# Kernel tuning notes

Measured on AMD Instinct MI355X. Metric: run time of the kernel, lower is better.

The kernel has to match this reference:

```python
import jax, jax.numpy as jnp
import numpy as np

DIM = 1024
NUM_HEADS = 16
HEAD_DIM = DIM // NUM_HEADS
SCALE = HEAD_DIM ** -0.5


def setup_inputs() -> dict:
    key = jax.random.key(0)
    k1, k2, k3 = jax.random.split(key, 3)
    B, S = 2, 2048
    x = jax.random.normal(k1, (B, S, DIM), dtype=jnp.float32)
    # nn.Linear(dim, 3*dim, bias=False): store as [in, out] for x @ W
    w_qkv = jax.random.normal(k2, (DIM, 3 * DIM), dtype=jnp.float32) * (DIM ** -0.5)
    w_out = jax.random.normal(k3, (DIM, DIM), dtype=jnp.float32) * (DIM ** -0.5)
    return {"x": x, "w_qkv": w_qkv, "w_out": w_out}


def reference(x, w_qkv, w_out):
    B, S, _ = x.shape
    qkv = x @ w_qkv                               # [B,S,3*D]
    q, k, v = jnp.split(qkv, 3, axis=-1)          # each [B,S,D]
    def heads(t):
        return t.reshape(B, S, NUM_HEADS, HEAD_DIM).transpose(0, 2, 1, 3)  # [B,H,S,d]
    q, k, v = heads(q), heads(k), heads(v)
    scores = jnp.einsum('bhqd,bhkd->bhqk', q, k) * SCALE   # [B,H,S,S]
    probs = jax.nn.softmax(scores, axis=-1)
    out = jnp.einsum('bhqk,bhkd->bhqd', probs, v)          # [B,H,S,d]
    out = out.transpose(0, 2, 1, 3).reshape(B, S, DIM)
    return out @ w_out
```

## Files before the change

### kernel.cpp

```cpp
#include <hip/hip_runtime.h>


typedef __bf16 bf16x8 __attribute__((ext_vector_type(8)));
typedef __bf16 bf16x4 __attribute__((ext_vector_type(4)));
typedef float floatx4 __attribute__((ext_vector_type(4)));
typedef _Float16 f16x4 __attribute__((ext_vector_type(4)));
typedef _Float16 f16x8 __attribute__((ext_vector_type(8)));

#define MFMA16(a, b, c) __builtin_amdgcn_mfma_f32_16x16x32_bf16((a), (b), (c), 0, 0, 0)

__device__ __forceinline__ void gl_lds16(const void* g, void* l) {
  __builtin_amdgcn_global_load_lds((__attribute__((address_space(1))) void*)(g),
                                   (__attribute__((address_space(3))) void*)(l),
                                   16, 0, 0);
}

__global__ __launch_bounds__(256) void prep(const float* __restrict__ x,
                                            const float* __restrict__ w_qkv,
                                            const float* __restrict__ w_out,
                                            __bf16* __restrict__ xb,
                                            __bf16* __restrict__ wqkvt,
                                            __bf16* __restrict__ woutt) {
  __shared__ float tile[64][65];
  const int bid = blockIdx.x, t = threadIdx.x;
  if (bid < 4096) {
    int i = (bid * 256 + t) * 4;
    float4 v = *(const float4*)(x + i);
    bf16x4 o = { (__bf16)v.x, (__bf16)v.y, (__bf16)v.z, (__bf16)v.w };
    *(bf16x4*)(xb + i) = o;
    return;
  }
  const float* w;
  __bf16* wt;
  int K = 1024, N, k0, n0;
  if (bid < 4864) {
    int i = bid - 4096;
    w = w_qkv; wt = wqkvt; N = 3072; k0 = (i & 15) * 64; n0 = (i >> 4) * 64;
  } else {
    int i = bid - 4864;
    w = w_out; wt = woutt; N = 1024; k0 = (i & 15) * 64; n0 = (i >> 4) * 64;
  }
  for (int j = 0; j < 16; ++j) {
    int e = j * 256 + t, r = e >> 6, c = e & 63;
    tile[r][c] = w[(size_t)(k0 + r) * N + n0 + c];
  }
  __syncthreads();
  for (int j = 0; j < 16; ++j) {
    int e = j * 256 + t, r = e >> 6, c = e & 63;
    wt[(size_t)(n0 + r) * K + k0 + c] = (__bf16)tile[c][r];
  }
}

__global__ __launch_bounds__(256) void gemm_qkv(const __bf16* __restrict__ A,
                                                const __bf16* __restrict__ Bt,
                                                __bf16* __restrict__ qkb,
                                                __bf16* __restrict__ vt) {
  constexpr int K = 1024;
  __shared__ __align__(16) __bf16 aS[128 * 32];
  __shared__ __align__(16) __bf16 bS[128 * 32];
  const int t = threadIdx.x;
  const int lane = t & 63, wave = t >> 6;
  const int l15 = lane & 15, quad = lane >> 4;
  const int wm = wave >> 1, wn = wave & 1;
  const int m0 = blockIdx.y * 128, n0 = blockIdx.x * 128;

  const floatx4 fzero = {0.f, 0.f, 0.f, 0.f};
  floatx4 acc[4][4];
  for (int mt = 0; mt < 4; ++mt)
    for (int nt = 0; nt < 4; ++nt) acc[mt][nt] = fzero;

  const int arow = t >> 2;
  const int ach = ((t & 3) ^ (arow & 3)) * 8;
  const __bf16* gA0 = A + (size_t)(m0 + arow) * K + ach;
  const __bf16* gA1 = gA0 + (size_t)64 * K;
  const __bf16* gB0 = Bt + (size_t)(n0 + arow) * K + ach;
  const __bf16* gB1 = gB0 + (size_t)64 * K;
  const int swz = (quad ^ (l15 & 3)) * 8;

  for (int k0 = 0; k0 < K; k0 += 32) {
    __syncthreads();
    gl_lds16(gA0 + k0, (char*)aS + t * 16);
    gl_lds16(gA1 + k0, (char*)aS + 4096 + t * 16);
    gl_lds16(gB0 + k0, (char*)bS + t * 16);
    gl_lds16(gB1 + k0, (char*)bS + 4096 + t * 16);
    __syncthreads();

    bf16x8 af[4], bfr[4];
    for (int mt = 0; mt < 4; ++mt)
      af[mt] = *(const bf16x8*)(aS + (wm * 64 + mt * 16 + l15) * 32 + swz);
    for (int nt = 0; nt < 4; ++nt)
      bfr[nt] = *(const bf16x8*)(bS + (wn * 64 + nt * 16 + l15) * 32 + swz);
    for (int mt = 0; mt < 4; ++mt)
      for (int nt = 0; nt < 4; ++nt)
        acc[mt][nt] = MFMA16(af[mt], bfr[nt], acc[mt][nt]);
  }

  for (int mt = 0; mt < 4; ++mt) {
    int row = m0 + wm * 64 + mt * 16 + quad * 4;
    for (int nt = 0; nt < 4; ++nt) {
      int col0 = n0 + wn * 64 + nt * 16;
      if (col0 >= 2048) {
        int dfull = col0 + l15 - 2048;
        int bh = ((row >> 11) << 4) + (dfull >> 6);
        int d = dfull & 63, s0 = row & 2047;
        bf16x4 pk = { (__bf16)acc[mt][nt][0], (__bf16)acc[mt][nt][1],
                      (__bf16)acc[mt][nt][2], (__bf16)acc[mt][nt][3] };
        *(bf16x4*)(vt + ((size_t)bh * 64 + d) * 2048 + s0) = pk;
      } else {
        int col = col0 + l15;
        __bf16* cp = qkb + (size_t)row * 2048 + col;
        for (int r = 0; r < 4; ++r) cp[(size_t)r * 2048] = (__bf16)acc[mt][nt][r];
      }
    }
  }
}

__global__ __launch_bounds__(256) void gemm_n64(const __bf16* __restrict__ A,
                                                const __bf16* __restrict__ Bt,
                                                float* __restrict__ C) {
  constexpr int K = 1024, N = 1024;
  __shared__ __align__(16) __bf16 aS[128 * 32];
  __shared__ __align__(16) __bf16 bS[64 * 32];
  const int t = threadIdx.x;
  const int lane = t & 63, wave = t >> 6;
  const int l15 = lane & 15, quad = lane >> 4;
  const int m0 = blockIdx.y * 128, n0 = blockIdx.x * 64;

  const floatx4 fzero = {0.f, 0.f, 0.f, 0.f};
  floatx4 acc[2][4];
  for (int mt = 0; mt < 2; ++mt)
    for (int nt = 0; nt < 4; ++nt) acc[mt][nt] = fzero;

  const int arow = t >> 2;
  const int ach = ((t & 3) ^ (arow & 3)) * 8;
  const __bf16* gA0 = A + (size_t)(m0 + arow) * K + ach;
  const __bf16* gA1 = gA0 + (size_t)64 * K;
  const __bf16* gB0 = Bt + (size_t)(n0 + arow) * K + ach;
  const int swz = (quad ^ (l15 & 3)) * 8;

  for (int k0 = 0; k0 < K; k0 += 32) {
    __syncthreads();
    gl_lds16(gA0 + k0, (char*)aS + t * 16);
    gl_lds16(gA1 + k0, (char*)aS + 4096 + t * 16);
    gl_lds16(gB0 + k0, (char*)bS + t * 16);
    __syncthreads();

    bf16x8 af[2], bfr[4];
    for (int mt = 0; mt < 2; ++mt)
      af[mt] = *(const bf16x8*)(aS + (wave * 32 + mt * 16 + l15) * 32 + swz);
    for (int nt = 0; nt < 4; ++nt)
      bfr[nt] = *(const bf16x8*)(bS + (nt * 16 + l15) * 32 + swz);
    for (int mt = 0; mt < 2; ++mt)
      for (int nt = 0; nt < 4; ++nt)
        acc[mt][nt] = MFMA16(af[mt], bfr[nt], acc[mt][nt]);
  }

  for (int mt = 0; mt < 2; ++mt) {
    int row = m0 + wave * 32 + mt * 16 + quad * 4;
    for (int nt = 0; nt < 4; ++nt) {
      int col = n0 + nt * 16 + l15;
      float* cp = C + (size_t)row * N + col;
      for (int r = 0; r < 4; ++r) cp[(size_t)r * N] = acc[mt][nt][r];
    }
  }
}

__global__ __launch_bounds__(256) void flash_attn(const __bf16* __restrict__ qkb,
                                                  const __bf16* __restrict__ vt,
                                                  _Float16* __restrict__ oPart,
                                                  float* __restrict__ lPart) {
  constexpr float SCALE = 0.125f;
  __shared__ __align__(16) __bf16 kS[2 * 64 * 64];
  __shared__ __align__(16) __bf16 vS[2 * 64 * 64];
  __shared__ __align__(16) __bf16 pT[4 * 16 * 64];

  const int t = threadIdx.x;
  const int lane = t & 63, wave = t >> 6;
  const int l15 = lane & 15, quad = lane >> 4;
  const int qb = blockIdx.x, bh = blockIdx.y, grp = blockIdx.z;
  const int b = bh >> 4, h = bh & 15;

  bf16x8 qf[2][2];
  for (int qt = 0; qt < 2; ++qt) {
    const __bf16* qp = qkb +
        (size_t)(b * 2048 + qb * 128 + wave * 32 + qt * 16 + l15) * 2048 + h * 64 + quad * 8;
    qf[qt][0] = *(const bf16x8*)qp;
    qf[qt][1] = *(const bf16x8*)(qp + 32);
  }

  const floatx4 fzero = {0.f, 0.f, 0.f, 0.f};
  floatx4 oacc[2][4];
  float lsum[2] = {0.f, 0.f};
  for (int qt = 0; qt < 2; ++qt)
    for (int dt = 0; dt < 4; ++dt) oacc[qt][dt] = fzero;

  const int srow = t >> 3, schk = (t & 7) ^ (srow & 7);
  const __bf16* kg0 =
      qkb + (size_t)(b * 2048 + grp * 1024 + srow) * 2048 + 1024 + h * 64 + schk * 8;
  const __bf16* kg1 = kg0 + (size_t)32 * 2048;
  const __bf16* vg0 =
      vt + (size_t)bh * 64 * 2048 + (size_t)srow * 2048 + grp * 1024 + schk * 8;
  const __bf16* vg1 = vg0 + (size_t)32 * 2048;

  const int l7 = l15 & 7;
  __bf16* pw = pT + wave * 1024 + l15 * 64;

  gl_lds16(kg0, (char*)kS + t * 16);
  gl_lds16(kg1, (char*)kS + 4096 + t * 16);
  gl_lds16(vg0, (char*)vS + t * 16);
  gl_lds16(vg1, (char*)vS + 4096 + t * 16);

  for (int nb = 0; nb < 16; ++nb) {
    __syncthreads();

    if (nb < 15) {
      const size_t n1 = (size_t)(nb + 1) * 64;
      const int oB = ((nb + 1) & 1) * 8192;
      gl_lds16(kg0 + n1 * 2048, (char*)kS + oB + t * 16);
      gl_lds16(kg1 + n1 * 2048, (char*)kS + oB + 4096 + t * 16);
      gl_lds16(vg0 + n1, (char*)vS + oB + t * 16);
      gl_lds16(vg1 + n1, (char*)vS + oB + 4096 + t * 16);
    }

    const __bf16* kC = kS + (nb & 1) * 4096;
    const __bf16* vC = vS + (nb & 1) * 4096;

    bf16x8 kf[4][2];
    for (int nt = 0; nt < 4; ++nt)
      for (int ks = 0; ks < 2; ++ks)
        kf[nt][ks] = *(const bf16x8*)(kC + (nt * 16 + l15) * 64 +
                                      ((ks * 4 + quad) ^ l7) * 8);
    bf16x8 vf[2][4];
    for (int ks = 0; ks < 2; ++ks)
      for (int dt = 0; dt < 4; ++dt)
        vf[ks][dt] = *(const bf16x8*)(vC + (dt * 16 + l15) * 64 +
                                      ((ks * 4 + quad) ^ l7) * 8);

    for (int qt = 0; qt < 2; ++qt) {
      floatx4 sa[4];
      for (int nt = 0; nt < 4; ++nt) {
        floatx4 a = fzero;
        a = MFMA16(kf[nt][0], qf[qt][0], a);
        a = MFMA16(kf[nt][1], qf[qt][1], a);
        sa[nt] = a;
      }
      float ls = 0.f;
      for (int nt = 0; nt < 4; ++nt) {
        float p0 = __expf(sa[nt][0] * SCALE);
        float p1 = __expf(sa[nt][1] * SCALE);
        float p2 = __expf(sa[nt][2] * SCALE);
        float p3 = __expf(sa[nt][3] * SCALE);
        ls += (p0 + p1) + (p2 + p3);
        bf16x4 pk = { (__bf16)p0, (__bf16)p1, (__bf16)p2, (__bf16)p3 };
        *(bf16x4*)(pw + ((nt * 2 + (quad >> 1)) ^ l7) * 8 + (quad & 1) * 4) = pk;
      }
      lsum[qt] += ls;
      for (int ks = 0; ks < 2; ++ks) {
        bf16x8 pa = *(const bf16x8*)(pw + ((ks * 4 + quad) ^ l7) * 8);
        for (int dt = 0; dt < 4; ++dt)
          oacc[qt][dt] = MFMA16(pa, vf[ks][dt], oacc[qt][dt]);
      }
    }
  }

  _Float16* oP = oPart + (size_t)grp * 4096 * 1024;
  float* lP = lPart + (size_t)grp * 4096 * 16;
  for (int qt = 0; qt < 2; ++qt) {
    float ls = lsum[qt];
    ls += __shfl_xor(ls, 16);
    ls += __shfl_xor(ls, 32);
    int rowb = qb * 128 + wave * 32 + qt * 16;
    if (quad == 0)
      lP[(size_t)(b * 2048 + rowb + l15) * 16 + h] = ls;
    _Float16* ob = oP + (size_t)(b * 2048 + rowb + quad * 4) * 1024 + h * 64;
    for (int dt = 0; dt < 4; ++dt)
      for (int r = 0; r < 4; ++r)
        ob[(size_t)r * 1024 + dt * 16 + l15] = (_Float16)oacc[qt][dt][r];
  }
}

__global__ __launch_bounds__(256) void combine(const _Float16* __restrict__ oPart,
                                               const float* __restrict__ lPart,
                                               __bf16* __restrict__ aout) {
  size_t i = ((size_t)blockIdx.x * 256 + threadIdx.x) * 8;
  int row = i >> 10, h = (i >> 6) & 15;
  float l0 = lPart[(size_t)row * 16 + h];
  float l1 = lPart[(size_t)4096 * 16 + (size_t)row * 16 + h];
  float inv = 1.f / (l0 + l1);
  f16x8 a = *(const f16x8*)(oPart + i);
  f16x8 c = *(const f16x8*)(oPart + (size_t)4096 * 1024 + i);
  bf16x8 o;
  for (int j = 0; j < 8; ++j) o[j] = (__bf16)(((float)a[j] + (float)c[j]) * inv);
  *(bf16x8*)(aout + i) = o;
}

extern "C" void kernel_launch(void* const* d_in, const int* in_sizes, int n_in,
                              void* d_out, int out_size, void* d_ws, size_t ws_size,
                              hipStream_t stream) {
  const float* x = (const float*)d_in[0];
  const float* w_qkv = (const float*)d_in[1];
  const float* w_out = (const float*)d_in[2];
  float* out = (float*)d_out;

  char* ws = (char*)d_ws;
  __bf16* xb = (__bf16*)(ws);
  __bf16* wqkvt = (__bf16*)(ws + ((size_t)8 << 20));
  _Float16* oPart = (_Float16*)(ws);
  __bf16* qkb = (__bf16*)(ws + ((size_t)16 << 20));
  __bf16* vtg = (__bf16*)(ws + ((size_t)32 << 20));
  __bf16* aout = (__bf16*)(ws + ((size_t)40 << 20));
  __bf16* woutt = (__bf16*)(ws + ((size_t)48 << 20));
  float* lPart = (float*)(ws + ((size_t)50 << 20));

  prep<<<5120, 256, 0, stream>>>(x, w_qkv, w_out, xb, wqkvt, woutt);
  gemm_qkv<<<dim3(24, 32), 256, 0, stream>>>(xb, wqkvt, qkb, vtg);
  flash_attn<<<dim3(16, 32, 2), 256, 0, stream>>>(qkb, vtg, oPart, lPart);
  combine<<<2048, 256, 0, stream>>>(oPart, lPart, aout);
  gemm_n64<<<dim3(16, 32), 256, 0, stream>>>(aout, woutt, out);
}
```

Measured before the change: 206.5 us.

## Drop split-KV attention and combine kernel; fold scale into Q and use exp2

Flash attention now runs over the full key range in a single block per (head, query tile), normalizing in-kernel and writing bf16 directly. This removes the separate combine kernel and the fp16 partial buffers. The softmax scale times log2(e) is folded into Q in the QKV GEMM epilogue so the kernel can use a raw exp2. Row sums are computed with an extra MFMA against a ones vector instead of VALU adds and shuffles. Blocks are remapped so heads group by XCD for better L2 reuse. The trade-off is half as many blocks (512), which lowers parallelism, and the loop is twice as long with no max-subtraction, so stability relies on small scores.

```diff
diff --git a/kernel.cpp b/kernel.cpp
--- a/kernel.cpp
+++ b/kernel.cpp
@@ -4,10 +4,27 @@
 typedef __bf16 bf16x8 __attribute__((ext_vector_type(8)));
 typedef __bf16 bf16x4 __attribute__((ext_vector_type(4)));
 typedef float floatx4 __attribute__((ext_vector_type(4)));
-typedef _Float16 f16x4 __attribute__((ext_vector_type(4)));
-typedef _Float16 f16x8 __attribute__((ext_vector_type(8)));
 
 #define MFMA16(a, b, c) __builtin_amdgcn_mfma_f32_16x16x32_bf16((a), (b), (c), 0, 0, 0)
+
+#if defined(__has_builtin)
+#if __has_builtin(__builtin_amdgcn_exp2f)
+#define EXP2F __builtin_amdgcn_exp2f
+#endif
+#endif
+#ifndef EXP2F
+#define EXP2F exp2f
+#endif
+
+__device__ __forceinline__ unsigned pk_bf16(float a, float b) {
+  union { float f; unsigned u; } ua, ub;
+  ua.f = a; ub.f = b;
+#if defined(__has_builtin) && __has_builtin(__builtin_amdgcn_perm)
+  return __builtin_amdgcn_perm(ub.u + 0x8000u, ua.u + 0x8000u, 0x07060302u);
+#else
+  return ((ua.u + 0x8000u) >> 16) | ((ub.u + 0x8000u) & 0xFFFF0000u);
+#endif
+}
 
 __device__ __forceinline__ void gl_lds16(const void* g, void* l) {
   __builtin_amdgcn_global_load_lds((__attribute__((address_space(1))) void*)(g),
@@ -56,6 +73,7 @@
                                                 __bf16* __restrict__ qkb,
                                                 __bf16* __restrict__ vt) {
   constexpr int K = 1024;
+  constexpr float QSCALE = 0.18033688f;
   __shared__ __align__(16) __bf16 aS[128 * 32];
   __shared__ __align__(16) __bf16 bS[128 * 32];
   const int t = threadIdx.x;
@@ -107,9 +125,10 @@
                       (__bf16)acc[mt][nt][2], (__bf16)acc[mt][nt][3] };
         *(bf16x4*)(vt + ((size_t)bh * 64 + d) * 2048 + s0) = pk;
       } else {
+        float sc = (col0 < 1024) ? QSCALE : 1.0f;
         int col = col0 + l15;
         __bf16* cp = qkb + (size_t)row * 2048 + col;
-        for (int r = 0; r < 4; ++r) cp[(size_t)r * 2048] = (__bf16)acc[mt][nt][r];
+        for (int r = 0; r < 4; ++r) cp[(size_t)r * 2048] = (__bf16)(acc[mt][nt][r] * sc);
       }
     }
   }
@@ -167,9 +186,7 @@
 
 __global__ __launch_bounds__(256) void flash_attn(const __bf16* __restrict__ qkb,
                                                   const __bf16* __restrict__ vt,
-                                                  _Float16* __restrict__ oPart,
-                                                  float* __restrict__ lPart) {
-  constexpr float SCALE = 0.125f;
+                                                  __bf16* __restrict__ out) {
   __shared__ __align__(16) __bf16 kS[2 * 64 * 64];
   __shared__ __align__(16) __bf16 vS[2 * 64 * 64];
   __shared__ __align__(16) __bf16 pT[4 * 16 * 64];
@@ -177,7 +194,9 @@
   const int t = threadIdx.x;
   const int lane = t & 63, wave = t >> 6;
   const int l15 = lane & 15, quad = lane >> 4;
-  const int qb = blockIdx.x, bh = blockIdx.y, grp = blockIdx.z;
+  const int id = blockIdx.x;
+  const int xcd = id & 7, slot = id >> 3;
+  const int bh = xcd * 4 + (slot >> 4), qb = slot & 15;
   const int b = bh >> 4, h = bh & 15;
 
   bf16x8 qf[2][2];
@@ -188,18 +207,22 @@
     qf[qt][1] = *(const bf16x8*)(qp + 32);
   }
 
+  bf16x8 onef;
+  for (int j = 0; j < 8; ++j) onef[j] = (__bf16)1.0f;
+
   const floatx4 fzero = {0.f, 0.f, 0.f, 0.f};
-  floatx4 oacc[2][4];
-  float lsum[2] = {0.f, 0.f};
-  for (int qt = 0; qt < 2; ++qt)
+  floatx4 oacc[2][4], lacc[2];
+  for (int qt = 0; qt < 2; ++qt) {
+    lacc[qt] = fzero;
     for (int dt = 0; dt < 4; ++dt) oacc[qt][dt] = fzero;
+  }
 
   const int srow = t >> 3, schk = (t & 7) ^ (srow & 7);
   const __bf16* kg0 =
-      qkb + (size_t)(b * 2048 + grp * 1024 + srow) * 2048 + 1024 + h * 64 + schk * 8;
+      qkb + (size_t)(b * 2048 + srow) * 2048 + 1024 + h * 64 + schk * 8;
   const __bf16* kg1 = kg0 + (size_t)32 * 2048;
   const __bf16* vg0 =
-      vt + (size_t)bh * 64 * 2048 + (size_t)srow * 2048 + grp * 1024 + schk * 8;
+      vt + (size_t)bh * 64 * 2048 + (size_t)srow * 2048 + schk * 8;
   const __bf16* vg1 = vg0 + (size_t)32 * 2048;
 
   const int l7 = l15 & 7;
@@ -210,10 +233,10 @@
   gl_lds16(vg0, (char*)vS + t * 16);
   gl_lds16(vg1, (char*)vS + 4096 + t * 16);
 
-  for (int nb = 0; nb < 16; ++nb) {
-    __syncthreads();
-
-    if (nb < 15) {
+  for (int nb = 0; nb < 32; ++nb) {
+    __syncthreads();
+
+    if (nb < 31) {
       const size_t n1 = (size_t)(nb + 1) * 64;
       const int oB = ((nb + 1) & 1) * 8192;
       gl_lds16(kg0 + n1 * 2048, (char*)kS + oB + t * 16);
@@ -244,54 +267,34 @@
         a = MFMA16(kf[nt][1], qf[qt][1], a);
         sa[nt] = a;
       }
-      float ls = 0.f;
       for (int nt = 0; nt < 4; ++nt) {
-        float p0 = __expf(sa[nt][0] * SCALE);
-        float p1 = __expf(sa[nt][1] * SCALE);
-        float p2 = __expf(sa[nt][2] * SCALE);
-        float p3 = __expf(sa[nt][3] * SCALE);
-        ls += (p0 + p1) + (p2 + p3);
-        bf16x4 pk = { (__bf16)p0, (__bf16)p1, (__bf16)p2, (__bf16)p3 };
-        *(bf16x4*)(pw + ((nt * 2 + (quad >> 1)) ^ l7) * 8 + (quad & 1) * 4) = pk;
+        float p0 = EXP2F(sa[nt][0]);
+        float p1 = EXP2F(sa[nt][1]);
+        float p2 = EXP2F(sa[nt][2]);
+        float p3 = EXP2F(sa[nt][3]);
+        unsigned w0 = pk_bf16(p0, p1);
+        unsigned w1 = pk_bf16(p2, p3);
+        uint2 wv = {w0, w1};
+        *(uint2*)((char*)pw + (((nt * 2 + (quad >> 1)) ^ l7) * 16 + (quad & 1) * 8)) = wv;
       }
-      lsum[qt] += ls;
       for (int ks = 0; ks < 2; ++ks) {
         bf16x8 pa = *(const bf16x8*)(pw + ((ks * 4 + quad) ^ l7) * 8);
         for (int dt = 0; dt < 4; ++dt)
           oacc[qt][dt] = MFMA16(pa, vf[ks][dt], oacc[qt][dt]);
+        lacc[qt] = MFMA16(pa, onef, lacc[qt]);
       }
     }
   }
 
-  _Float16* oP = oPart + (size_t)grp * 4096 * 1024;
-  float* lP = lPart + (size_t)grp * 4096 * 16;
   for (int qt = 0; qt < 2; ++qt) {
-    float ls = lsum[qt];
-    ls += __shfl_xor(ls, 16);
-    ls += __shfl_xor(ls, 32);
-    int rowb = qb * 128 + wave * 32 + qt * 16;
-    if (quad == 0)
-      lP[(size_t)(b * 2048 + rowb + l15) * 16 + h] = ls;
-    _Float16* ob = oP + (size_t)(b * 2048 + rowb + quad * 4) * 1024 + h * 64;
+    float inv[4];
+    for (int r = 0; r < 4; ++r) inv[r] = 1.f / lacc[qt][r];
+    __bf16* ob = out +
+        (size_t)(b * 2048 + qb * 128 + wave * 32 + qt * 16 + quad * 4) * 1024 + h * 64;
     for (int dt = 0; dt < 4; ++dt)
       for (int r = 0; r < 4; ++r)
-        ob[(size_t)r * 1024 + dt * 16 + l15] = (_Float16)oacc[qt][dt][r];
-  }
-}
-
-__global__ __launch_bounds__(256) void combine(const _Float16* __restrict__ oPart,
-                                               const float* __restrict__ lPart,
-                                               __bf16* __restrict__ aout) {
-  size_t i = ((size_t)blockIdx.x * 256 + threadIdx.x) * 8;
-  int row = i >> 10, h = (i >> 6) & 15;
-  float l0 = lPart[(size_t)row * 16 + h];
-  float l1 = lPart[(size_t)4096 * 16 + (size_t)row * 16 + h];
-  float inv = 1.f / (l0 + l1);
-  f16x8 a = *(const f16x8*)(oPart + i);
-  f16x8 c = *(const f16x8*)(oPart + (size_t)4096 * 1024 + i);
-  bf16x8 o;
-  for (int j = 0; j < 8; ++j) o[j] = (__bf16)(((float)a[j] + (float)c[j]) * inv);
-  *(bf16x8*)(aout + i) = o;
+        ob[(size_t)r * 1024 + dt * 16 + l15] = (__bf16)(oacc[qt][dt][r] * inv[r]);
+  }
 }
 
 extern "C" void kernel_launch(void* const* d_in, const int* in_sizes, int n_in,
@@ -305,16 +308,13 @@
   char* ws = (char*)d_ws;
   __bf16* xb = (__bf16*)(ws);
   __bf16* wqkvt = (__bf16*)(ws + ((size_t)8 << 20));
-  _Float16* oPart = (_Float16*)(ws);
   __bf16* qkb = (__bf16*)(ws + ((size_t)16 << 20));
   __bf16* vtg = (__bf16*)(ws + ((size_t)32 << 20));
   __bf16* aout = (__bf16*)(ws + ((size_t)40 << 20));
   __bf16* woutt = (__bf16*)(ws + ((size_t)48 << 20));
-  float* lPart = (float*)(ws + ((size_t)50 << 20));
 
   prep<<<5120, 256, 0, stream>>>(x, w_qkv, w_out, xb, wqkvt, woutt);
   gemm_qkv<<<dim3(24, 32), 256, 0, stream>>>(xb, wqkvt, qkb, vtg);
-  flash_attn<<<dim3(16, 32, 2), 256, 0, stream>>>(qkb, vtg, oPart, lPart);
-  combine<<<2048, 256, 0, stream>>>(oPart, lPart, aout);
+  flash_attn<<<512, 256, 0, stream>>>(qkb, vtg, aout);
   gemm_n64<<<dim3(16, 32), 256, 0, stream>>>(aout, woutt, out);
 }
```

Result: faster. 190.6 us (-7.7%).
